# Kernel tuning notes

Hardware: AMD Instinct MI355X
Metric: run time of the kernel (lower is better)

The kernel has to match this reference:

```python
import jax, jax.numpy as jnp
import numpy as np

N_EMBD = 1024
N_HEAD = 16
HEAD_DIM = N_EMBD // N_HEAD
LN_EPS = 1e-5


def setup_inputs() -> dict:
    key = jax.random.key(0)
    ks = jax.random.split(key, 8)
    B, T, C = 4, 2048, N_EMBD
    s = lambda fan_in: 1.0 / np.sqrt(fan_in)
    return {
        'x': jax.random.normal(ks[0], (B, T, C), dtype=jnp.float32),
        'w_qkv': jax.random.normal(ks[1], (C, 3 * C), dtype=jnp.float32) * s(C),
        'b_qkv': jnp.zeros((3 * C,), dtype=jnp.float32),
        'ln1_g': jnp.ones((C,), dtype=jnp.float32),
        'ln1_b': jnp.zeros((C,), dtype=jnp.float32),
        'w_fc1': jax.random.normal(ks[2], (C, 4 * C), dtype=jnp.float32) * s(C),
        'b_fc1': jnp.zeros((4 * C,), dtype=jnp.float32),
        'w_fc2': jax.random.normal(ks[3], (4 * C, C), dtype=jnp.float32) * s(4 * C),
        'b_fc2': jnp.zeros((C,), dtype=jnp.float32),
        'ln2_g': jnp.ones((C,), dtype=jnp.float32),
        'ln2_b': jnp.zeros((C,), dtype=jnp.float32),
    }


def _layernorm(x, g, b):
    mu = jnp.mean(x, axis=-1, keepdims=True)
    var = jnp.mean(jnp.square(x - mu), axis=-1, keepdims=True)
    return (x - mu) * jax.lax.rsqrt(var + LN_EPS) * g + b


def _attention(x, w_qkv, b_qkv):
    B, T, C = x.shape
    qkv = x @ w_qkv + b_qkv                      # [B,T,3C]
    q, k, v = jnp.split(qkv, 3, axis=-1)
    q = q.reshape(B, T, N_HEAD, HEAD_DIM)
    k = k.reshape(B, T, N_HEAD, HEAD_DIM)
    v = v.reshape(B, T, N_HEAD, HEAD_DIM)
    scores = jnp.einsum('bqhd,bkhd->bhqk', q, k) / np.sqrt(HEAD_DIM).astype(np.float32)
    causal = jnp.tril(jnp.ones((T, T), dtype=bool))
    scores = jnp.where(causal, scores, -jnp.inf)
    attn = jax.nn.softmax(scores, axis=-1)       # [B,H,T,T]
    y = jnp.einsum('bhqk,bkhd->bqhd', attn, v)
    return y.reshape(B, T, C)


def reference(x, w_qkv, b_qkv, ln1_g, ln1_b, w_fc1, b_fc1, w_fc2, b_fc2, ln2_g, ln2_b):
    # Block: x = ln1(x + attn(x)); x = ln2(x + mlp(x))   (post-LN residual)
    x = _layernorm(x + _attention(x, w_qkv, b_qkv), ln1_g, ln1_b)
    h = jax.nn.gelu(x @ w_fc1 + b_fc1, approximate=False)
    mlp = h @ w_fc2 + b_fc2
    x = _layernorm(x + mlp, ln2_g, ln2_b)
    return x
```

## Files before the change

kernel.cpp:

```cpp
#include <hip/hip_runtime.h>
#include <cstdint>
#include <cstddef>

#define TB 4
#define TT 2048
#define TC 1024
#define NH 16
#define HD 64
#define MROWS (TB * TT)

typedef __bf16 bf16;
typedef unsigned short u16;
typedef __bf16 bf16x8 __attribute__((ext_vector_type(8)));
typedef float floatx4 __attribute__((ext_vector_type(4)));
typedef unsigned short ushort8 __attribute__((ext_vector_type(8)));
typedef unsigned short ushort4v __attribute__((ext_vector_type(4)));

#define LOG2E 1.4426950408889634f

static __device__ __forceinline__ u16 f2bfbits(float f) {
    bf16 b = (bf16)f;
    return __builtin_bit_cast(u16, b);
}

#if __has_builtin(__builtin_amdgcn_exp2f)
#define EXP2F(x) __builtin_amdgcn_exp2f(x)
#else
#define EXP2F(x) exp2f(x)
#endif

static __device__ __forceinline__ void gld_lds16(const u16* g, const u16* lds) {
    __builtin_amdgcn_global_load_lds(
        (const __attribute__((address_space(1))) unsigned int*)(uintptr_t)g,
        (__attribute__((address_space(3))) unsigned int*)(unsigned int)(uintptr_t)lds,
        16, 0, 0);
}

__global__ __launch_bounds__(256) void prep_kernel(
    const float* __restrict__ x, u16* __restrict__ xb,
    const float* __restrict__ w_qkv, u16* __restrict__ wqkvT,
    const float* __restrict__ w_fc1, u16* __restrict__ wfc1T,
    const float* __restrict__ w_fc2, u16* __restrict__ wfc2T)
{
    const int tid = threadIdx.x;
    int blk = blockIdx.x;
    if (blk < 8192) {
        const int i = blk * 256 + tid;
        float4 v = reinterpret_cast<const float4*>(x)[i];
        ushort4v o;
        o.x = f2bfbits(v.x); o.y = f2bfbits(v.y); o.z = f2bfbits(v.z); o.w = f2bfbits(v.w);
        reinterpret_cast<ushort4v*>(xb)[i] = o;
        return;
    }
    blk -= 8192;
    const float* in; u16* out; int K, N, bx, by;
    if (blk < 3072)      { in = w_qkv; out = wqkvT; K = TC;     N = 3 * TC; bx = blk % 96;  by = blk / 96; }
    else if (blk < 7168) { blk -= 3072; in = w_fc1; out = wfc1T; K = TC;    N = 4 * TC; bx = blk & 127; by = blk >> 7; }
    else                 { blk -= 7168; in = w_fc2; out = wfc2T; K = 4 * TC; N = TC;    bx = blk & 31;  by = blk >> 5; }
    __shared__ float tile[32][33];
    const int n0 = bx * 32, k0 = by * 32;
    const int tx = tid & 31, ty = tid >> 5;
    for (int r = 0; r < 32; r += 8)
        tile[ty + r][tx] = in[(size_t)(k0 + ty + r) * N + n0 + tx];
    __syncthreads();
    for (int r = 0; r < 32; r += 8)
        out[(size_t)(n0 + ty + r) * K + k0 + tx] = f2bfbits(tile[tx][ty + r]);
}

template <int GELU>
__global__ __launch_bounds__(256, 2) void gemm_bt_kernel(
    const u16* __restrict__ A, const u16* __restrict__ Bt,
    const float* __restrict__ bias, u16* __restrict__ Cmat,
    int Nb, int Ksz)
{
    __shared__ u16 As[128 * 64];
    __shared__ u16 Bs[256 * 64];
    const int tid  = threadIdx.x;
    const int wave = tid >> 6, lane = tid & 63;
    const int quad = lane >> 4, l16 = lane & 15;
    const int Nsz = Nb * 256;
    const int bid = blockIdx.x;
    const int xcd = bid & 7, qb = bid >> 3;
    const int m0 = (xcd * 8 + qb / Nb) * 128;
    const int n0 = (qb % Nb) * 256;
    const int wm = (wave >> 1) * 64, wn = (wave & 1) * 128;

    const int srow = lane >> 3;
    const int scol = ((lane & 7) ^ srow) * 8;
    const u16* ap = A  + (size_t)(m0 + wave * 32 + srow) * Ksz + scol;
    const u16* bp = Bt + (size_t)(n0 + wave * 8  + srow) * Ksz + scol;
    const size_t astep = (size_t)8  * Ksz;
    const size_t bstep = (size_t)32 * Ksz;

    floatx4 acc[4][8];
#pragma unroll
    for (int i = 0; i < 4; i++)
#pragma unroll
        for (int j = 0; j < 8; j++)
            acc[i][j] = (floatx4){0.f, 0.f, 0.f, 0.f};

    const int l7 = l16 & 7;

    for (int k0 = 0; k0 < Ksz; k0 += 64) {
        __syncthreads();
#pragma unroll
        for (int d = 0; d < 4; d++)
            gld_lds16(ap + d * astep, As + (wave * 4 + d) * 512);
#pragma unroll
        for (int d = 0; d < 8; d++)
            gld_lds16(bp + d * bstep, Bs + d * 2048 + wave * 512);
        ap += 64; bp += 64;
        __syncthreads();

#pragma unroll
        for (int t = 0; t < 2; t++) {
            const int po = ((t * 4 + quad) ^ l7) * 8;
            bf16x8 af[4], bfr[8];
#pragma unroll
            for (int i = 0; i < 4; i++)
                af[i] = *reinterpret_cast<const bf16x8*>(As + (wm + i * 16 + l16) * 64 + po);
#pragma unroll
            for (int j = 0; j < 8; j++)
                bfr[j] = *reinterpret_cast<const bf16x8*>(Bs + (wn + j * 16 + l16) * 64 + po);
#pragma unroll
            for (int i = 0; i < 4; i++)
#pragma unroll
                for (int j = 0; j < 8; j++)
                    acc[i][j] = __builtin_amdgcn_mfma_f32_16x16x32_bf16(af[i], bfr[j], acc[i][j], 0, 0, 0);
        }
    }

    float bv[8];
#pragma unroll
    for (int j = 0; j < 8; j++) bv[j] = bias[n0 + wn + j * 16 + l16];
    const int odd = l16 & 1;
#pragma unroll
    for (int i = 0; i < 4; i++) {
        const int row0 = m0 + wm + i * 16 + quad * 4;
#pragma unroll
        for (int j = 0; j < 8; j++) {
            float v[4];
#pragma unroll
            for (int r = 0; r < 4; r++) {
                float t = acc[i][j][r] + bv[j];
                if (GELU) {
                    float u = t * (0.7978845608f + 0.0356774081f * t * t);
                    float e = EXP2F(u * (2.0f * LOG2E));
                    t = t - t * __builtin_amdgcn_rcpf(e + 1.0f);
                }
                v[r] = t;
            }
            float pv0 = __shfl_xor(v[0], 1), pv1 = __shfl_xor(v[1], 1);
            float pv2 = __shfl_xor(v[2], 1), pv3 = __shfl_xor(v[3], 1);
            float lo0 = odd ? pv2 : v[0];
            float hi0 = odd ? v[2] : pv0;
            float lo1 = odd ? pv3 : v[1];
            float hi1 = odd ? v[3] : pv1;
            unsigned int d0 = (unsigned int)f2bfbits(lo0) | ((unsigned int)f2bfbits(hi0) << 16);
            unsigned int d1 = (unsigned int)f2bfbits(lo1) | ((unsigned int)f2bfbits(hi1) << 16);
            const int row  = row0 + odd * 2;
            const int colp = n0 + wn + j * 16 + (l16 & ~1);
            *reinterpret_cast<unsigned int*>(Cmat + (size_t)row * Nsz + colp)       = d0;
            *reinterpret_cast<unsigned int*>(Cmat + (size_t)(row + 1) * Nsz + colp) = d1;
        }
    }
}

template <int GELU>
__global__ __launch_bounds__(256, 2) void gemm_bt128_kernel(
    const u16* __restrict__ A, const u16* __restrict__ Bt,
    const float* __restrict__ bias, u16* __restrict__ Cmat,
    int Nb, int Ksz)
{
    __shared__ u16 As[128 * 64];
    __shared__ u16 Bs[128 * 64];
    const int tid  = threadIdx.x;
    const int wave = tid >> 6, lane = tid & 63;
    const int quad = lane >> 4, l16 = lane & 15;
    const int Nsz = Nb * 128;
    const int bid = blockIdx.x;
    const int xcd = bid & 7, qb = bid >> 3;
    const int m0 = (xcd * 8 + qb / Nb) * 128;
    const int n0 = (qb % Nb) * 128;
    const int wm = (wave >> 1) * 64, wn = (wave & 1) * 64;

    const int srow = lane >> 3;
    const int scol = ((lane & 7) ^ srow) * 8;
    const u16* ap = A  + (size_t)(m0 + wave * 32 + srow) * Ksz + scol;
    const u16* bp = Bt + (size_t)(n0 + wave * 32 + srow) * Ksz + scol;
    const size_t astep = (size_t)8 * Ksz;

    floatx4 acc[4][4];
#pragma unroll
    for (int i = 0; i < 4; i++)
#pragma unroll
        for (int j = 0; j < 4; j++)
            acc[i][j] = (floatx4){0.f, 0.f, 0.f, 0.f};

    const int l7 = l16 & 7;

    for (int k0 = 0; k0 < Ksz; k0 += 64) {
        __syncthreads();
#pragma unroll
        for (int d = 0; d < 4; d++)
            gld_lds16(ap + d * astep, As + (wave * 4 + d) * 512);
#pragma unroll
        for (int d = 0; d < 4; d++)
            gld_lds16(bp + d * astep, Bs + (wave * 4 + d) * 512);
        ap += 64; bp += 64;
        __syncthreads();

#pragma unroll
        for (int t = 0; t < 2; t++) {
            const int po = ((t * 4 + quad) ^ l7) * 8;
            bf16x8 af[4], bfr[4];
#pragma unroll
            for (int i = 0; i < 4; i++)
                af[i] = *reinterpret_cast<const bf16x8*>(As + (wm + i * 16 + l16) * 64 + po);
#pragma unroll
            for (int j = 0; j < 4; j++)
                bfr[j] = *reinterpret_cast<const bf16x8*>(Bs + (wn + j * 16 + l16) * 64 + po);
#pragma unroll
            for (int i = 0; i < 4; i++)
#pragma unroll
                for (int j = 0; j < 4; j++)
                    acc[i][j] = __builtin_amdgcn_mfma_f32_16x16x32_bf16(af[i], bfr[j], acc[i][j], 0, 0, 0);
        }
    }

    float bv[4];
#pragma unroll
    for (int j = 0; j < 4; j++) bv[j] = bias[n0 + wn + j * 16 + l16];
    const int odd = l16 & 1;
#pragma unroll
    for (int i = 0; i < 4; i++) {
        const int row0 = m0 + wm + i * 16 + quad * 4;
#pragma unroll
        for (int j = 0; j < 4; j++) {
            float v[4];
#pragma unroll
            for (int r = 0; r < 4; r++) {
                float t = acc[i][j][r] + bv[j];
                if (GELU) {
                    float u = t * (0.7978845608f + 0.0356774081f * t * t);
                    float e = EXP2F(u * (2.0f * LOG2E));
                    t = t - t * __builtin_amdgcn_rcpf(e + 1.0f);
                }
                v[r] = t;
            }
            float pv0 = __shfl_xor(v[0], 1), pv1 = __shfl_xor(v[1], 1);
            float pv2 = __shfl_xor(v[2], 1), pv3 = __shfl_xor(v[3], 1);
            float lo0 = odd ? pv2 : v[0];
            float hi0 = odd ? v[2] : pv0;
            float lo1 = odd ? pv3 : v[1];
            float hi1 = odd ? v[3] : pv1;
            unsigned int d0 = (unsigned int)f2bfbits(lo0) | ((unsigned int)f2bfbits(hi0) << 16);
            unsigned int d1 = (unsigned int)f2bfbits(lo1) | ((unsigned int)f2bfbits(hi1) << 16);
            const int row  = row0 + odd * 2;
            const int colp = n0 + wn + j * 16 + (l16 & ~1);
            *reinterpret_cast<unsigned int*>(Cmat + (size_t)row * Nsz + colp)       = d0;
            *reinterpret_cast<unsigned int*>(Cmat + (size_t)(row + 1) * Nsz + colp) = d1;
        }
    }
}

__global__ __launch_bounds__(512) void attn_kernel(const u16* __restrict__ qkv,
                                                   u16* __restrict__ y)
{
    __shared__ u16 Ks[2 * 64 * 64];
    __shared__ u16 Vt[2 * 64 * 64];
    __shared__ u16 Pw[8][16 * 64];
    const int tid  = threadIdx.x;
    const int wave = tid >> 6, lane = tid & 63;
    const int quad = lane >> 4, l16 = lane & 15;
    const int l7   = l16 & 7;
    const int h = blockIdx.y, b = blockIdx.z;
    const int rowbase = b * TT;
    const int S3C = 3 * TC;

    const int srow = (tid >> 3) & 31;
    const int c8   = (tid & 7) * 8;
    const int pcK  = ((tid & 7) ^ (srow & 7)) * 8;
    const int pvb  = (srow + ((tid & 7) << 2)) & 31;
    const bool kRole = (tid < 256);
    const int pcr = (quad ^ l7) * 8;
    unsigned int* const vtw = (unsigned int*)Vt;

    for (int pass = 0; pass < 2; pass++) {
        const int qt   = pass ? (15 - (int)blockIdx.x) : (int)blockIdx.x;
        const int q0b  = qt * 128;
        const int q0w  = q0b + wave * 16;
        const int kend = q0b + 128;

        __syncthreads();

        bf16x8 qf0, qf1;
        {
            const u16* qrow = qkv + (size_t)(rowbase + q0w + l16) * S3C + h * HD + quad * 8;
            bf16x8 t0 = *reinterpret_cast<const bf16x8*>(qrow);
            bf16x8 t1 = *reinterpret_cast<const bf16x8*>(qrow + 32);
#pragma unroll
            for (int i = 0; i < 8; i++) {
                t0[i] = (bf16)((float)t0[i] * (0.125f * LOG2E));
                t1[i] = (bf16)((float)t1[i] * (0.125f * LOG2E));
            }
            qf0 = t0; qf1 = t1;
        }

        float m_s = -__builtin_inff(), l_s = 0.f;
        floatx4 o_acc[4];
#pragma unroll
        for (int n = 0; n < 4; n++) o_acc[n] = (floatx4){0.f, 0.f, 0.f, 0.f};

        const u16* gp = kRole
            ? qkv + (size_t)(rowbase + srow) * S3C + TC + h * HD + c8
            : qkv + (size_t)(rowbase + 2 * srow) * S3C + 2 * TC + h * HD + c8;
        const size_t g2 = kRole ? (size_t)32 * S3C : (size_t)S3C;
        ushort8 r0 = *reinterpret_cast<const ushort8*>(gp);
        ushort8 r1 = *reinterpret_cast<const ushort8*>(gp + g2);

        int buf = 0;
        for (int k0 = 0; k0 < kend; k0 += 64) {
            if (kRole) {
                u16* kb = Ks + buf * 4096;
                *reinterpret_cast<ushort8*>(kb + srow * 64 + pcK)        = r0;
                *reinterpret_cast<ushort8*>(kb + (srow + 32) * 64 + pcK) = r1;
            } else {
                unsigned int* vb = vtw + buf * 2048;
#pragma unroll
                for (int j = 0; j < 8; j++) {
                    unsigned int pk = (unsigned int)r0[j] | ((unsigned int)r1[j] << 16);
                    vb[(c8 + j) * 32 + (pvb ^ (j << 2))] = pk;
                }
            }
            __syncthreads();

            if (k0 + 64 < kend) {
                const u16* gn = gp + (size_t)(k0 + 64) * S3C;
                r0 = *reinterpret_cast<const ushort8*>(gn);
                r1 = *reinterpret_cast<const ushort8*>(gn + g2);
            }

            if (k0 <= q0w + 15) {
                const u16* ksb = Ks + buf * 4096;
                floatx4 st[4];
#pragma unroll
                for (int t = 0; t < 4; t++) {
                    const u16* krowp = ksb + (t * 16 + l16) * 64;
                    bf16x8 ka  = *reinterpret_cast<const bf16x8*>(krowp + pcr);
                    bf16x8 kb2 = *reinterpret_cast<const bf16x8*>(krowp + (pcr ^ 32));
                    floatx4 s = (floatx4){0.f, 0.f, 0.f, 0.f};
                    s = __builtin_amdgcn_mfma_f32_16x16x32_bf16(ka, qf0, s, 0, 0, 0);
                    s = __builtin_amdgcn_mfma_f32_16x16x32_bf16(kb2, qf1, s, 0, 0, 0);
                    st[t] = s;
                }
                float v[16];
                if (k0 + 63 > q0w) {
                    const int kq = k0 - q0w;
#pragma unroll
                    for (int t = 0; t < 4; t++)
#pragma unroll
                        for (int r = 0; r < 4; r++)
                            v[t * 4 + r] = (t * 16 + quad * 4 + r + kq > l16)
                                               ? -__builtin_inff() : st[t][r];
                } else {
#pragma unroll
                    for (int t = 0; t < 4; t++)
#pragma unroll
                        for (int r = 0; r < 4; r++)
                            v[t * 4 + r] = st[t][r];
                }
                float mx = v[0];
#pragma unroll
                for (int i = 1; i < 16; i++) mx = fmaxf(mx, v[i]);
                mx = fmaxf(mx, __shfl_xor(mx, 16));
                mx = fmaxf(mx, __shfl_xor(mx, 32));
                const float mnew  = fmaxf(m_s, mx);
                const float alpha = EXP2F(m_s - mnew);
                float rs = 0.f;
                u16* const pwb = Pw[wave] + l16 * 64;
#pragma unroll
                for (int t = 0; t < 4; t++) {
                    float p0 = EXP2F(v[t * 4 + 0] - mnew);
                    float p1 = EXP2F(v[t * 4 + 1] - mnew);
                    float p2 = EXP2F(v[t * 4 + 2] - mnew);
                    float p3 = EXP2F(v[t * 4 + 3] - mnew);
                    rs += (p0 + p1) + (p2 + p3);
                    ushort4v pk;
                    pk.x = f2bfbits(p0); pk.y = f2bfbits(p1);
                    pk.z = f2bfbits(p2); pk.w = f2bfbits(p3);
                    *reinterpret_cast<ushort4v*>(
                        pwb + ((2 * t + (quad >> 1)) ^ l7) * 8 + (quad & 1) * 4) = pk;
                }
                rs += __shfl_xor(rs, 16);
                rs += __shfl_xor(rs, 32);
                l_s = l_s * alpha + rs;
                m_s = mnew;
#pragma unroll
                for (int n = 0; n < 4; n++) o_acc[n] *= alpha;

                bf16x8 pf0 = *reinterpret_cast<const bf16x8*>(pwb + pcr);
                bf16x8 pf1 = *reinterpret_cast<const bf16x8*>(pwb + (pcr ^ 32));
                const unsigned int* vbb = vtw + buf * 2048;
#pragma unroll
                for (int n = 0; n < 4; n++) {
                    const int dr  = n * 16 + l16;
                    const int pd0 = ((4 * (quad + 2 * n + (l16 >> 3))) & 31) ^ (l7 << 2);
                    bf16x8 vf0 = *reinterpret_cast<const bf16x8*>(vbb + dr * 32 + pd0);
                    bf16x8 vf1 = *reinterpret_cast<const bf16x8*>(vbb + dr * 32 + (pd0 ^ 16));
                    o_acc[n] = __builtin_amdgcn_mfma_f32_16x16x32_bf16(vf0, pf0, o_acc[n], 0, 0, 0);
                    o_acc[n] = __builtin_amdgcn_mfma_f32_16x16x32_bf16(vf1, pf1, o_acc[n], 0, 0, 0);
                }
            }
            buf ^= 1;
        }

        const float li = 1.0f / l_s;
        u16* yrow = y + (size_t)(rowbase + q0w + l16) * TC + h * HD;
#pragma unroll
        for (int n = 0; n < 4; n++) {
            ushort4v ov;
            ov.x = f2bfbits(o_acc[n][0] * li);
            ov.y = f2bfbits(o_acc[n][1] * li);
            ov.z = f2bfbits(o_acc[n][2] * li);
            ov.w = f2bfbits(o_acc[n][3] * li);
            *reinterpret_cast<ushort4v*>(yrow + n * 16 + quad * 4) = ov;
        }
    }
}

template <typename AT, typename OT>
__global__ __launch_bounds__(256) void ln_kernel(
    const AT* __restrict__ a, const bf16* __restrict__ bres,
    const float* __restrict__ g, const float* __restrict__ be,
    OT* __restrict__ out)
{
    const int row = blockIdx.x;
    const int tid = threadIdx.x;
    const size_t base = (size_t)row * TC;
    float v[4];
    for (int i = 0; i < 4; i++) {
        const int c = tid + i * 256;
        v[i] = (float)a[base + c] + (float)bres[base + c];
    }
    float s  = v[0] + v[1] + v[2] + v[3];
    float sq = v[0]*v[0] + v[1]*v[1] + v[2]*v[2] + v[3]*v[3];
    for (int off = 32; off >= 1; off >>= 1) {
        s  += __shfl_xor(s, off, 64);
        sq += __shfl_xor(sq, off, 64);
    }
    __shared__ float red[8];
    const int wv = tid >> 6, lane = tid & 63;
    if (lane == 0) { red[wv] = s; red[4 + wv] = sq; }
    __syncthreads();
    s  = red[0] + red[1] + red[2] + red[3];
    sq = red[4] + red[5] + red[6] + red[7];
    const float mu   = s * (1.0f / TC);
    const float var  = sq * (1.0f / TC) - mu * mu;
    const float rsig = rsqrtf(var + 1e-5f);
    for (int i = 0; i < 4; i++) {
        const int c = tid + i * 256;
        out[base + c] = (OT)((v[i] - mu) * rsig * g[c] + be[c]);
    }
}

extern "C" void kernel_launch(void* const* d_in, const int* in_sizes, int n_in,
                              void* d_out, int out_size, void* d_ws, size_t ws_size,
                              hipStream_t stream)
{
    const float* x     = (const float*)d_in[0];
    const float* w_qkv = (const float*)d_in[1];
    const float* b_qkv = (const float*)d_in[2];
    const float* ln1_g = (const float*)d_in[3];
    const float* ln1_b = (const float*)d_in[4];
    const float* w_fc1 = (const float*)d_in[5];
    const float* b_fc1 = (const float*)d_in[6];
    const float* w_fc2 = (const float*)d_in[7];
    const float* b_fc2 = (const float*)d_in[8];
    const float* ln2_g = (const float*)d_in[9];
    const float* ln2_b = (const float*)d_in[10];
    float* out = (float*)d_out;

    char* ws = (char*)d_ws;
    const size_t MB = 1ull << 20;
    u16* xb    = (u16*)(ws + 0);
    u16* wqkvT = (u16*)(ws + 16 * MB);
    u16* wfc1T = (u16*)(ws + 22 * MB);
    u16* wfc2T = (u16*)(ws + 30 * MB);
    u16* qkv   = (u16*)(ws + 38 * MB);
    u16* yb    = (u16*)(ws + 86 * MB);
    u16* x1    = (u16*)(ws + 102 * MB);
    u16* hb    = (u16*)(ws + 118 * MB);
    u16* mlp   = (u16*)(ws + 38 * MB);

    prep_kernel<<<19456, 256, 0, stream>>>(x, xb, w_qkv, wqkvT, w_fc1, wfc1T, w_fc2, wfc2T);

    gemm_bt_kernel<0><<<12 * 64, 256, 0, stream>>>(xb, wqkvT, b_qkv, qkv, 12, TC);
    attn_kernel<<<dim3(8, NH, TB), 512, 0, stream>>>(qkv, yb);
    ln_kernel<float, bf16><<<MROWS, 256, 0, stream>>>(x, (const bf16*)yb, ln1_g, ln1_b, (bf16*)x1);
    gemm_bt_kernel<1><<<16 * 64, 256, 0, stream>>>((const u16*)x1, wfc1T, b_fc1, hb, 16, TC);
    gemm_bt128_kernel<0><<<8 * 64, 256, 0, stream>>>(hb, wfc2T, b_fc2, mlp, 8, 4 * TC);
    ln_kernel<bf16, float><<<MROWS, 256, 0, stream>>>(
        (const bf16*)x1, (const bf16*)mlp, ln2_g, ln2_b, out);
}
```

Baseline: 417.4 us.

## Replace QKV/FC1 GEMM with 256x256 tile, 8-wave, double-buffered pipelined kernel

The 128x256 single-buffered GEMM used for the QKV and FC1 projections is replaced by a 512-thread kernel with 256x256 output tiles. It splits each 64-wide K step into halves and double-buffers them in LDS, issuing global-to-LDS loads for upcoming stages while MFMAs run. Explicit waitcnt, barrier and setprio calls interleave loads and compute, with a new swizzle for the 32-wide rows. The larger tile raises operand reuse and the pipelining hides load latency, at the cost of 128KB of LDS per block, fewer blocks per CU and fragile hand scheduling.

```diff
diff --git a/kernel.cpp b/kernel.cpp
--- a/kernel.cpp
+++ b/kernel.cpp
@@ -68,77 +68,104 @@
 }
 
 template <int GELU>
-__global__ __launch_bounds__(256, 2) void gemm_bt_kernel(
+__global__ __launch_bounds__(512, 2) void gemm256_kernel(
     const u16* __restrict__ A, const u16* __restrict__ Bt,
     const float* __restrict__ bias, u16* __restrict__ Cmat,
-    int Nb, int Ksz)
+    int Nb, int Mt, int Ksz)
 {
-    __shared__ u16 As[128 * 64];
-    __shared__ u16 Bs[256 * 64];
+    __shared__ u16 As[4 * 8192];
+    __shared__ u16 Bs[4 * 8192];
     const int tid  = threadIdx.x;
     const int wave = tid >> 6, lane = tid & 63;
     const int quad = lane >> 4, l16 = lane & 15;
+    const int wm = (wave >> 2) * 128, wn = (wave & 3) * 64;
     const int Nsz = Nb * 256;
     const int bid = blockIdx.x;
     const int xcd = bid & 7, qb = bid >> 3;
-    const int m0 = (xcd * 8 + qb / Nb) * 128;
+    const int m0 = (xcd * (Mt >> 3) + qb / Nb) * 256;
     const int n0 = (qb % Nb) * 256;
-    const int wm = (wave >> 1) * 64, wn = (wave & 1) * 128;
-
-    const int srow = lane >> 3;
-    const int scol = ((lane & 7) ^ srow) * 8;
-    const u16* ap = A  + (size_t)(m0 + wave * 32 + srow) * Ksz + scol;
-    const u16* bp = Bt + (size_t)(n0 + wave * 8  + srow) * Ksz + scol;
-    const size_t astep = (size_t)8  * Ksz;
-    const size_t bstep = (size_t)32 * Ksz;
-
-    floatx4 acc[4][8];
-#pragma unroll
-    for (int i = 0; i < 4; i++)
-#pragma unroll
-        for (int j = 0; j < 8; j++)
+
+    const int srow = tid >> 2;
+    const int sc8  = ((tid & 3) ^ ((tid >> 3) & 3)) * 8;
+    const u16* aP = A  + (size_t)(m0 + srow) * Ksz + sc8;
+    const u16* bP = Bt + (size_t)(n0 + srow) * Ksz + sc8;
+    const size_t half2 = (size_t)128 * Ksz;
+    const int sdst = wave * 512;
+
+    const int slot = quad ^ ((l16 >> 1) & 3);
+    const int aRd = (wm + l16) * 32 + slot * 8;
+    const int bRd = (wn + l16) * 32 + slot * 8;
+
+    floatx4 acc[8][4];
+#pragma unroll
+    for (int i = 0; i < 8; i++)
+#pragma unroll
+        for (int j = 0; j < 4; j++)
             acc[i][j] = (floatx4){0.f, 0.f, 0.f, 0.f};
 
-    const int l7 = l16 & 7;
-
-    for (int k0 = 0; k0 < Ksz; k0 += 64) {
-        __syncthreads();
-#pragma unroll
-        for (int d = 0; d < 4; d++)
-            gld_lds16(ap + d * astep, As + (wave * 4 + d) * 512);
-#pragma unroll
-        for (int d = 0; d < 8; d++)
-            gld_lds16(bp + d * bstep, Bs + d * 2048 + wave * 512);
-        ap += 64; bp += 64;
-        __syncthreads();
-
-#pragma unroll
-        for (int t = 0; t < 2; t++) {
-            const int po = ((t * 4 + quad) ^ l7) * 8;
-            bf16x8 af[4], bfr[8];
-#pragma unroll
-            for (int i = 0; i < 4; i++)
-                af[i] = *reinterpret_cast<const bf16x8*>(As + (wm + i * 16 + l16) * 64 + po);
-#pragma unroll
-            for (int j = 0; j < 8; j++)
-                bfr[j] = *reinterpret_cast<const bf16x8*>(Bs + (wn + j * 16 + l16) * 64 + po);
-#pragma unroll
-            for (int i = 0; i < 4; i++)
-#pragma unroll
-                for (int j = 0; j < 8; j++)
-                    acc[i][j] = __builtin_amdgcn_mfma_f32_16x16x32_bf16(af[i], bfr[j], acc[i][j], 0, 0, 0);
-        }
-    }
-
-    float bv[8];
-#pragma unroll
-    for (int j = 0; j < 8; j++) bv[j] = bias[n0 + wn + j * 16 + l16];
+    const int nt = Ksz >> 6;
+
+#define SA(g, kh) do { const u16* s_ = aP + (g) * 64 + (kh) * 32; \
+    u16* d_ = As + (((g) & 1) * 2 + (kh)) * 8192 + sdst; \
+    gld_lds16(s_, d_); gld_lds16(s_ + half2, d_ + 4096); } while (0)
+#define SB(g, kh) do { const u16* s_ = bP + (g) * 64 + (kh) * 32; \
+    u16* d_ = Bs + (((g) & 1) * 2 + (kh)) * 8192 + sdst; \
+    gld_lds16(s_, d_); gld_lds16(s_ + half2, d_ + 4096); } while (0)
+
+    SA(0, 0); SB(0, 0); SA(0, 1); SB(0, 1); SA(1, 0); SB(1, 0);
+    asm volatile("s_waitcnt vmcnt(4)" ::: "memory");
+    __builtin_amdgcn_sched_barrier(0);
+    __builtin_amdgcn_s_barrier();
+
+#define PHASE(CH, KH, STAGE_STMT, TAILWAIT) do { \
+    const u16* ab_ = As + (p * 2 + (KH)) * 8192 + aRd + (CH) * 2048; \
+    const u16* bb_ = Bs + (p * 2 + (KH)) * 8192 + bRd; \
+    bf16x8 af_[4], bf_[4]; \
+    _Pragma("unroll") \
+    for (int i_ = 0; i_ < 4; i_++) \
+        af_[i_] = *reinterpret_cast<const bf16x8*>(ab_ + i_ * 512); \
+    _Pragma("unroll") \
+    for (int j_ = 0; j_ < 4; j_++) \
+        bf_[j_] = *reinterpret_cast<const bf16x8*>(bb_ + j_ * 512); \
+    STAGE_STMT; \
+    __builtin_amdgcn_s_barrier(); \
+    asm volatile("s_waitcnt lgkmcnt(0)" ::: "memory"); \
+    __builtin_amdgcn_sched_barrier(0); \
+    __builtin_amdgcn_s_setprio(1); \
+    _Pragma("unroll") \
+    for (int i_ = 0; i_ < 4; i_++) \
+    _Pragma("unroll") \
+    for (int j_ = 0; j_ < 4; j_++) \
+        acc[(CH) * 4 + i_][j_] = __builtin_amdgcn_mfma_f32_16x16x32_bf16( \
+            af_[i_], bf_[j_], acc[(CH) * 4 + i_][j_], 0, 0, 0); \
+    __builtin_amdgcn_s_setprio(0); \
+    TAILWAIT; \
+    __builtin_amdgcn_s_barrier(); \
+} while (0)
+
+    for (int g = 0; g < nt; ++g) {
+        const int p = g & 1;
+        PHASE(0, 0, if (g + 1 < nt) SA(g + 1, 1), );
+        PHASE(1, 0, if (g + 1 < nt) SB(g + 1, 1), );
+        PHASE(1, 1, if (g + 2 < nt) SA(g + 2, 0), );
+        PHASE(0, 1, if (g + 2 < nt) SB(g + 2, 0),
+              if (g < nt - 2) { asm volatile("s_waitcnt vmcnt(4)" ::: "memory"); }
+              else           { asm volatile("s_waitcnt vmcnt(0)" ::: "memory"); }
+              __builtin_amdgcn_sched_barrier(0));
+    }
+#undef PHASE
+#undef SA
+#undef SB
+
+    float bv[4];
+#pragma unroll
+    for (int j = 0; j < 4; j++) bv[j] = bias[n0 + wn + j * 16 + l16];
     const int odd = l16 & 1;
 #pragma unroll
-    for (int i = 0; i < 4; i++) {
+    for (int i = 0; i < 8; i++) {
         const int row0 = m0 + wm + i * 16 + quad * 4;
 #pragma unroll
-        for (int j = 0; j < 8; j++) {
+        for (int j = 0; j < 4; j++) {
             float v[4];
 #pragma unroll
             for (int r = 0; r < 4; r++) {
@@ -495,10 +522,10 @@
 
     prep_kernel<<<19456, 256, 0, stream>>>(x, xb, w_qkv, wqkvT, w_fc1, wfc1T, w_fc2, wfc2T);
 
-    gemm_bt_kernel<0><<<12 * 64, 256, 0, stream>>>(xb, wqkvT, b_qkv, qkv, 12, TC);
+    gemm256_kernel<0><<<384, 512, 0, stream>>>(xb, wqkvT, b_qkv, qkv, 12, 32, TC);
     attn_kernel<<<dim3(8, NH, TB), 512, 0, stream>>>(qkv, yb);
     ln_kernel<float, bf16><<<MROWS, 256, 0, stream>>>(x, (const bf16*)yb, ln1_g, ln1_b, (bf16*)x1);
-    gemm_bt_kernel<1><<<16 * 64, 256, 0, stream>>>((const u16*)x1, wfc1T, b_fc1, hb, 16, TC);
+    gemm256_kernel<1><<<512, 512, 0, stream>>>((const u16*)x1, wfc1T, b_fc1, hb, 16, 32, TC);
     gemm_bt128_kernel<0><<<8 * 64, 256, 0, stream>>>(hb, wfc2T, b_fc2, mlp, 8, 4 * TC);
     ln_kernel<bf16, float><<<MROWS, 256, 0, stream>>>(
         (const bf16*)x1, (const bf16*)mlp, ln2_g, ln2_b, out);
```

New measurement: 439.0 us. +5.2%, slower.

## Software-pipeline GEMM k-loop with split-K halves and double-buffered LDS

Applied to the files above, without the earlier changes.

Rewrites the three GEMM main loops so each 64-wide K tile is split into two 32-wide halves held in separate LDS buffers. The async global-to-LDS loads for the next tile's half are issued while MFMAs run on the current half, ordered with explicit vmcnt/lgkmcnt waits, raw barriers and sched_barrier fences. It also raises wave priority around the MFMA bursts and changes the LDS swizzle for the 32-wide rows. The goal is to hide global load latency behind compute instead of stalling at a barrier after every load. In exchange there are more barriers per tile, and correctness depends on hand-counted wait values.

```diff
diff --git a/kernel.cpp b/kernel.cpp
--- a/kernel.cpp
+++ b/kernel.cpp
@@ -35,6 +35,8 @@
         (__attribute__((address_space(3))) unsigned int*)(unsigned int)(uintptr_t)lds,
         16, 0, 0);
 }
+
+#define SBAR0 __builtin_amdgcn_sched_barrier(0)
 
 __global__ __launch_bounds__(256) void prep_kernel(
     const float* __restrict__ x, u16* __restrict__ xb,
@@ -68,13 +70,13 @@
 }
 
 template <int GELU>
-__global__ __launch_bounds__(256, 2) void gemm_bt_kernel(
+__global__ __launch_bounds__(256, 2) void gemm_pl_kernel(
     const u16* __restrict__ A, const u16* __restrict__ Bt,
     const float* __restrict__ bias, u16* __restrict__ Cmat,
     int Nb, int Ksz)
 {
-    __shared__ u16 As[128 * 64];
-    __shared__ u16 Bs[256 * 64];
+    __shared__ u16 As[2][128 * 32];
+    __shared__ u16 Bs[2][256 * 32];
     const int tid  = threadIdx.x;
     const int wave = tid >> 6, lane = tid & 63;
     const int quad = lane >> 4, l16 = lane & 15;
@@ -85,12 +87,15 @@
     const int n0 = (qb % Nb) * 256;
     const int wm = (wave >> 1) * 64, wn = (wave & 1) * 128;
 
-    const int srow = lane >> 3;
-    const int scol = ((lane & 7) ^ srow) * 8;
-    const u16* ap = A  + (size_t)(m0 + wave * 32 + srow) * Ksz + scol;
-    const u16* bp = Bt + (size_t)(n0 + wave * 8  + srow) * Ksz + scol;
-    const size_t astep = (size_t)8  * Ksz;
-    const size_t bstep = (size_t)32 * Ksz;
+    const int sc8 = ((tid & 3) ^ ((tid >> 3) & 3)) * 8;
+    const u16* aP = A  + (size_t)(m0 + (tid >> 2)) * Ksz + sc8;
+    const u16* bP = Bt + (size_t)(n0 + (tid >> 2)) * Ksz + sc8;
+    const size_t rstep = (size_t)64 * Ksz;
+    const int sdst = wave * 512;
+
+    const int slot = quad ^ ((l16 >> 1) & 3);
+    const int aRd = (wm + l16) * 32 + slot * 8;
+    const int bRd = (wn + l16) * 32 + slot * 8;
 
     floatx4 acc[4][8];
 #pragma unroll
@@ -99,36 +104,65 @@
         for (int j = 0; j < 8; j++)
             acc[i][j] = (floatx4){0.f, 0.f, 0.f, 0.f};
 
-    const int l7 = l16 & 7;
-
-    for (int k0 = 0; k0 < Ksz; k0 += 64) {
-        __syncthreads();
-#pragma unroll
-        for (int d = 0; d < 4; d++)
-            gld_lds16(ap + d * astep, As + (wave * 4 + d) * 512);
-#pragma unroll
-        for (int d = 0; d < 8; d++)
-            gld_lds16(bp + d * bstep, Bs + d * 2048 + wave * 512);
-        ap += 64; bp += 64;
-        __syncthreads();
-
-#pragma unroll
-        for (int t = 0; t < 2; t++) {
-            const int po = ((t * 4 + quad) ^ l7) * 8;
-            bf16x8 af[4], bfr[8];
-#pragma unroll
-            for (int i = 0; i < 4; i++)
-                af[i] = *reinterpret_cast<const bf16x8*>(As + (wm + i * 16 + l16) * 64 + po);
-#pragma unroll
-            for (int j = 0; j < 8; j++)
-                bfr[j] = *reinterpret_cast<const bf16x8*>(Bs + (wn + j * 16 + l16) * 64 + po);
-#pragma unroll
-            for (int i = 0; i < 4; i++)
-#pragma unroll
-                for (int j = 0; j < 8; j++)
-                    acc[i][j] = __builtin_amdgcn_mfma_f32_16x16x32_bf16(af[i], bfr[j], acc[i][j], 0, 0, 0);
-        }
-    }
+    const int nt = Ksz >> 6;
+
+#define SSTG(g, kh) do { \
+    const u16* as_ = aP + (size_t)(g) * 64 + (kh) * 32; \
+    _Pragma("unroll") \
+    for (int d_ = 0; d_ < 2; d_++) \
+        gld_lds16(as_ + d_ * rstep, &As[kh][0] + d_ * 2048 + sdst); \
+    const u16* bs_ = bP + (size_t)(g) * 64 + (kh) * 32; \
+    _Pragma("unroll") \
+    for (int d_ = 0; d_ < 4; d_++) \
+        gld_lds16(bs_ + d_ * rstep, &Bs[kh][0] + d_ * 2048 + sdst); } while (0)
+
+#define RD(kh) do { \
+    const u16* ab_ = &As[kh][0] + aRd; \
+    const u16* bb_ = &Bs[kh][0] + bRd; \
+    _Pragma("unroll") \
+    for (int i_ = 0; i_ < 4; i_++) af[i_] = *reinterpret_cast<const bf16x8*>(ab_ + i_ * 512); \
+    _Pragma("unroll") \
+    for (int j_ = 0; j_ < 8; j_++) bfr[j_] = *reinterpret_cast<const bf16x8*>(bb_ + j_ * 512); } while (0)
+
+#define MM() do { \
+    __builtin_amdgcn_s_setprio(1); \
+    _Pragma("unroll") \
+    for (int i_ = 0; i_ < 4; i_++) \
+    _Pragma("unroll") \
+    for (int j_ = 0; j_ < 8; j_++) \
+        acc[i_][j_] = __builtin_amdgcn_mfma_f32_16x16x32_bf16( \
+            af[i_], bfr[j_], acc[i_][j_], 0, 0, 0); \
+    __builtin_amdgcn_s_setprio(0); } while (0)
+
+    SSTG(0, 0); SSTG(0, 1);
+    asm volatile("s_waitcnt vmcnt(6)" ::: "memory");
+    SBAR0; __builtin_amdgcn_s_barrier(); SBAR0;
+
+    for (int g = 0; g < nt; ++g) {
+        bf16x8 af[4], bfr[8];
+        RD(0);
+        asm volatile("s_waitcnt lgkmcnt(0)" ::: "memory");
+        SBAR0; __builtin_amdgcn_s_barrier(); SBAR0;
+        if (g + 1 < nt) SSTG(g + 1, 0);
+        SBAR0;
+        MM();
+        if (g + 1 < nt) { asm volatile("s_waitcnt vmcnt(6)" ::: "memory"); }
+        else            { asm volatile("s_waitcnt vmcnt(0)" ::: "memory"); }
+        SBAR0; __builtin_amdgcn_s_barrier(); SBAR0;
+        RD(1);
+        asm volatile("s_waitcnt lgkmcnt(0)" ::: "memory");
+        SBAR0; __builtin_amdgcn_s_barrier(); SBAR0;
+        if (g + 1 < nt) SSTG(g + 1, 1);
+        SBAR0;
+        MM();
+        if (g + 1 < nt) {
+            asm volatile("s_waitcnt vmcnt(6)" ::: "memory");
+            SBAR0; __builtin_amdgcn_s_barrier(); SBAR0;
+        }
+    }
+#undef MM
+#undef RD
+#undef SSTG
 
     float bv[8];
 #pragma unroll
@@ -167,13 +201,13 @@
 }
 
 template <int GELU>
-__global__ __launch_bounds__(256, 2) void gemm_bt128_kernel(
+__global__ __launch_bounds__(256, 2) void gemm_pl128_kernel(
     const u16* __restrict__ A, const u16* __restrict__ Bt,
     const float* __restrict__ bias, u16* __restrict__ Cmat,
     int Nb, int Ksz)
 {
-    __shared__ u16 As[128 * 64];
-    __shared__ u16 Bs[128 * 64];
+    __shared__ u16 As[2][128 * 32];
+    __shared__ u16 Bs[2][128 * 32];
     const int tid  = threadIdx.x;
     const int wave = tid >> 6, lane = tid & 63;
     const int quad = lane >> 4, l16 = lane & 15;
@@ -184,11 +218,15 @@
     const int n0 = (qb % Nb) * 128;
     const int wm = (wave >> 1) * 64, wn = (wave & 1) * 64;
 
-    const int srow = lane >> 3;
-    const int scol = ((lane & 7) ^ srow) * 8;
-    const u16* ap = A  + (size_t)(m0 + wave * 32 + srow) * Ksz + scol;
-    const u16* bp = Bt + (size_t)(n0 + wave * 32 + srow) * Ksz + scol;
-    const size_t astep = (size_t)8 * Ksz;
+    const int sc8 = ((tid & 3) ^ ((tid >> 3) & 3)) * 8;
+    const u16* aP = A  + (size_t)(m0 + (tid >> 2)) * Ksz + sc8;
+    const u16* bP = Bt + (size_t)(n0 + (tid >> 2)) * Ksz + sc8;
+    const size_t rstep = (size_t)64 * Ksz;
+    const int sdst = wave * 512;
+
+    const int slot = quad ^ ((l16 >> 1) & 3);
+    const int aRd = (wm + l16) * 32 + slot * 8;
+    const int bRd = (wn + l16) * 32 + slot * 8;
 
     floatx4 acc[4][4];
 #pragma unroll
@@ -197,36 +235,65 @@
         for (int j = 0; j < 4; j++)
             acc[i][j] = (floatx4){0.f, 0.f, 0.f, 0.f};
 
-    const int l7 = l16 & 7;
-
-    for (int k0 = 0; k0 < Ksz; k0 += 64) {
-        __syncthreads();
-#pragma unroll
-        for (int d = 0; d < 4; d++)
-            gld_lds16(ap + d * astep, As + (wave * 4 + d) * 512);
-#pragma unroll
-        for (int d = 0; d < 4; d++)
-            gld_lds16(bp + d * astep, Bs + (wave * 4 + d) * 512);
-        ap += 64; bp += 64;
-        __syncthreads();
-
-#pragma unroll
-        for (int t = 0; t < 2; t++) {
-            const int po = ((t * 4 + quad) ^ l7) * 8;
-            bf16x8 af[4], bfr[4];
-#pragma unroll
-            for (int i = 0; i < 4; i++)
-                af[i] = *reinterpret_cast<const bf16x8*>(As + (wm + i * 16 + l16) * 64 + po);
-#pragma unroll
-            for (int j = 0; j < 4; j++)
-                bfr[j] = *reinterpret_cast<const bf16x8*>(Bs + (wn + j * 16 + l16) * 64 + po);
-#pragma unroll
-            for (int i = 0; i < 4; i++)
-#pragma unroll
-                for (int j = 0; j < 4; j++)
-                    acc[i][j] = __builtin_amdgcn_mfma_f32_16x16x32_bf16(af[i], bfr[j], acc[i][j], 0, 0, 0);
-        }
-    }
+    const int nt = Ksz >> 6;
+
+#define SSTG(g, kh) do { \
+    const u16* as_ = aP + (size_t)(g) * 64 + (kh) * 32; \
+    _Pragma("unroll") \
+    for (int d_ = 0; d_ < 2; d_++) \
+        gld_lds16(as_ + d_ * rstep, &As[kh][0] + d_ * 2048 + sdst); \
+    const u16* bs_ = bP + (size_t)(g) * 64 + (kh) * 32; \
+    _Pragma("unroll") \
+    for (int d_ = 0; d_ < 2; d_++) \
+        gld_lds16(bs_ + d_ * rstep, &Bs[kh][0] + d_ * 2048 + sdst); } while (0)
+
+#define RD(kh) do { \
+    const u16* ab_ = &As[kh][0] + aRd; \
+    const u16* bb_ = &Bs[kh][0] + bRd; \
+    _Pragma("unroll") \
+    for (int i_ = 0; i_ < 4; i_++) af[i_] = *reinterpret_cast<const bf16x8*>(ab_ + i_ * 512); \
+    _Pragma("unroll") \
+    for (int j_ = 0; j_ < 4; j_++) bfr[j_] = *reinterpret_cast<const bf16x8*>(bb_ + j_ * 512); } while (0)
+
+#define MM() do { \
+    __builtin_amdgcn_s_setprio(1); \
+    _Pragma("unroll") \
+    for (int i_ = 0; i_ < 4; i_++) \
+    _Pragma("unroll") \
+    for (int j_ = 0; j_ < 4; j_++) \
+        acc[i_][j_] = __builtin_amdgcn_mfma_f32_16x16x32_bf16( \
+            af[i_], bfr[j_], acc[i_][j_], 0, 0, 0); \
+    __builtin_amdgcn_s_setprio(0); } while (0)
+
+    SSTG(0, 0); SSTG(0, 1);
+    asm volatile("s_waitcnt vmcnt(4)" ::: "memory");
+    SBAR0; __builtin_amdgcn_s_barrier(); SBAR0;
+
+    for (int g = 0; g < nt; ++g) {
+        bf16x8 af[4], bfr[4];
+        RD(0);
+        asm volatile("s_waitcnt lgkmcnt(0)" ::: "memory");
+        SBAR0; __builtin_amdgcn_s_barrier(); SBAR0;
+        if (g + 1 < nt) SSTG(g + 1, 0);
+        SBAR0;
+        MM();
+        if (g + 1 < nt) { asm volatile("s_waitcnt vmcnt(4)" ::: "memory"); }
+        else            { asm volatile("s_waitcnt vmcnt(0)" ::: "memory"); }
+        SBAR0; __builtin_amdgcn_s_barrier(); SBAR0;
+        RD(1);
+        asm volatile("s_waitcnt lgkmcnt(0)" ::: "memory");
+        SBAR0; __builtin_amdgcn_s_barrier(); SBAR0;
+        if (g + 1 < nt) SSTG(g + 1, 1);
+        SBAR0;
+        MM();
+        if (g + 1 < nt) {
+            asm volatile("s_waitcnt vmcnt(4)" ::: "memory");
+            SBAR0; __builtin_amdgcn_s_barrier(); SBAR0;
+        }
+    }
+#undef MM
+#undef RD
+#undef SSTG
 
     float bv[4];
 #pragma unroll
@@ -495,11 +562,11 @@
 
     prep_kernel<<<19456, 256, 0, stream>>>(x, xb, w_qkv, wqkvT, w_fc1, wfc1T, w_fc2, wfc2T);
 
-    gemm_bt_kernel<0><<<12 * 64, 256, 0, stream>>>(xb, wqkvT, b_qkv, qkv, 12, TC);
+    gemm_pl_kernel<0><<<12 * 64, 256, 0, stream>>>(xb, wqkvT, b_qkv, qkv, 12, TC);
     attn_kernel<<<dim3(8, NH, TB), 512, 0, stream>>>(qkv, yb);
     ln_kernel<float, bf16><<<MROWS, 256, 0, stream>>>(x, (const bf16*)yb, ln1_g, ln1_b, (bf16*)x1);
-    gemm_bt_kernel<1><<<16 * 64, 256, 0, stream>>>((const u16*)x1, wfc1T, b_fc1, hb, 16, TC);
-    gemm_bt128_kernel<0><<<8 * 64, 256, 0, stream>>>(hb, wfc2T, b_fc2, mlp, 8, 4 * TC);
+    gemm_pl_kernel<1><<<16 * 64, 256, 0, stream>>>((const u16*)x1, wfc1T, b_fc1, hb, 16, TC);
+    gemm_pl128_kernel<0><<<8 * 64, 256, 0, stream>>>(hb, wfc2T, b_fc2, mlp, 8, 4 * TC);
     ln_kernel<bf16, float><<<MROWS, 256, 0, stream>>>(
         (const bf16*)x1, (const bf16*)mlp, ln2_g, ln2_b, out);
 }
```

New measurement: 453.1 us. +8.5%, slower.
